# Kernel tuning notes

Measured on AMD Instinct MI355X. Metric: run time of the kernel, lower is better.

Reference implementation:

```python
import jax, jax.numpy as jnp
import numpy as np

B, T, H, C = 128, 1024, 512, 10


def setup_inputs() -> dict:
    key = jax.random.key(0)
    ks = jax.random.split(key, 8)
    s = 1.0 / np.sqrt(H)  # PyTorch LSTMCell/Linear default init scale
    return {
        "x": jax.random.normal(ks[0], (B, T), jnp.float32),
        "w_ih": jax.random.uniform(ks[1], (4 * H, 1), jnp.float32, -s, s),
        "w_hh": jax.random.uniform(ks[2], (4 * H, H), jnp.float32, -s, s),
        "b_ih": jax.random.uniform(ks[3], (4 * H,), jnp.float32, -s, s),
        "b_hh": jax.random.uniform(ks[4], (4 * H,), jnp.float32, -s, s),
        "w_t": jax.random.normal(ks[5], (2 * H, 1), jnp.float32) * 0.02,
        "w_fc": jax.random.uniform(ks[6], (C, H), jnp.float32, -s, s),
        "b_fc": jax.random.uniform(ks[7], (C,), jnp.float32, -s, s),
    }


def reference(x, w_ih, w_hh, b_ih, b_hh, w_t, w_fc, b_fc):
    # x: [B, T] scalar-per-step sequence (input_size == 1 in the original)
    Bz = x.shape[0]
    Hh = w_hh.shape[1]
    w1 = w_t[:Hh, 0]   # multiplies the new hidden h_t       [H]
    w2 = w_t[Hh:, 0]   # multiplies each history state h_j   [H]
    bias = b_ih + b_hh
    wih_row = w_ih[:, 0]  # [4H], since input_size == 1

    # Original computes, at step i, attn_c = sum_{j<=i} ((h_new@w1 + h_j@w2) * h_j)
    # over history [h_init=0, h_1, ..., h_i]. We keep running sums:
    #   S1 = sum_j h_j,   S2 = sum_j (h_j@w2) * h_j
    # so attn_c = (h_new@w1) * S1 + S2  -- identical math, O(T) instead of O(T^2).
    def step(carry, x_t):
        h, c, S1, S2 = carry
        gates = x_t[:, None] * wih_row[None, :] + h @ w_hh.T + bias  # [B,4H]
        i_g, f_g, g_g, o_g = jnp.split(gates, 4, axis=1)  # PyTorch gate order i,f,g,o
        c_new = jax.nn.sigmoid(f_g) * c + jax.nn.sigmoid(i_g) * jnp.tanh(g_g)
        h_new = jax.nn.sigmoid(o_g) * jnp.tanh(c_new)
        a = (h_new @ w1)[:, None]          # [B,1]
        attn = a * S1 + S2                 # [B,H]
        S1 = S1 + h_new
        S2 = S2 + (h_new @ w2)[:, None] * h_new
        return (h_new, c_new, S1, S2), (h_new, attn)

    z = jnp.zeros((Bz, Hh), x.dtype)
    _, (hs, attns) = jax.lax.scan(step, (z, z, z, z), x.T)  # [T,B,H] each
    out = jnp.transpose(hs + attns, (1, 0, 2))               # [B,T,H]
    return out @ w_fc.T + b_fc                               # [B,T,C]
```

## Files before the change

### kernel.cpp

```cpp
#include <hip/hip_runtime.h>
#include <math.h>

typedef __attribute__((ext_vector_type(8))) short bf16x8;
typedef __attribute__((ext_vector_type(4))) float f32x4;

static constexpr int Tt = 1024;
static constexpr int Hh = 512;
static constexpr int Cc = 10;

static constexpr int NXCD = 8;
static constexpr int BPX  = 32;
static constexpr int UPB  = 16;
static constexpr int NB   = 16;
static constexpr int THREADS = 256;
static constexpr int GRID = 256;

static constexpr size_t WS_HHI_B = 4096;
static constexpr size_t WS_HLO_B = 4096 + 32768;

__device__ __forceinline__ unsigned short f2bf(float f) {
    unsigned u = __builtin_bit_cast(unsigned, f);
    return (unsigned short)((u + 0x7FFFu + ((u >> 16) & 1u)) >> 16);
}
__device__ __forceinline__ float bf2f(unsigned short h) {
    unsigned u = ((unsigned)h) << 16;
    return __builtin_bit_cast(float, u);
}
__device__ __forceinline__ float dot4(float4 a, float4 b) {
    return a.x * b.x + a.y * b.y + a.z * b.z + a.w * b.w;
}
__device__ __forceinline__ float fsig(float x) {
    const float e = __builtin_amdgcn_exp2f(x * -1.44269504f);
    return __builtin_amdgcn_rcpf(1.0f + e);
}
__device__ __forceinline__ float ftanh(float x) {
    const float e = __builtin_amdgcn_exp2f(x * -2.88539008f);
    return 2.0f * __builtin_amdgcn_rcpf(1.0f + e) - 1.0f;
}

__global__ __launch_bounds__(THREADS, 1)
void lstm_fused(const float* __restrict__ x,
                const float* __restrict__ w_ih,
                const float* __restrict__ w_hh,
                const float* __restrict__ b_ih,
                const float* __restrict__ b_hh,
                const float* __restrict__ w_t,
                const float* __restrict__ w_fc,
                const float* __restrict__ b_fc,
                float* __restrict__ out,
                float* __restrict__ ws)
{
    const int tid  = threadIdx.x;
    const int lane = tid & 63;
    const int wv   = tid >> 6;

    int* flags    = (int*)ws;
    int* counters = (int*)ws + 256;
    unsigned short* hg_hi = (unsigned short*)((char*)ws + WS_HHI_B);
    unsigned short* hg_lo = (unsigned short*)((char*)ws + WS_HLO_B);

    __shared__ __align__(16) short wls_hi[64 * 512];
    __shared__ __align__(16) short wls_lo[64 * 512];
    __shared__ __align__(16) short hhi_ls[16 * 512];
    __shared__ __align__(16) short hlo_ls[16 * 512];
    float* gbuf = (float*)hhi_ls;
    int*   xchg = (int*)hlo_ls;

    if (tid == 0) {
        int xr;
        asm volatile("s_getreg_b32 %0, hwreg(20, 0, 32)" : "=s"(xr));
        const int xcd = xr & 7;
        xchg[0] = xcd;
        xchg[1] = atomicAdd(&counters[xcd * 32], 1) & 31;
    }
    __syncthreads();
    const int xcd  = xchg[0];
    const int rank = xchg[1];
    __syncthreads();
    const int fbase = xcd * BPX;

    {
        #pragma unroll
        for (int it = 0; it < 16; ++it) {
            const int idx = it * 256 + tid;
            const int lr = idx >> 6, kg = idx & 63;
            const int grow = (lr >> 4) * Hh + rank * UPB + (lr & 15);
            const float4* src = (const float4*)(w_hh + (size_t)grow * Hh + kg * 8);
            const float4 f0 = src[0], f1 = src[1];
            const float f[8] = { f0.x, f0.y, f0.z, f0.w, f1.x, f1.y, f1.z, f1.w };
            bf16x8 vhi, vlo;
            #pragma unroll
            for (int j = 0; j < 8; ++j) {
                const unsigned short h = f2bf(f[j]);
                vhi[j] = (short)h;
                vlo[j] = (short)f2bf(f[j] - bf2f(h));
            }
            const int off = (lr * 1024 + kg * 16) ^ ((lr & 7) << 4);
            *(bf16x8*)((char*)wls_hi + off) = vhi;
            *(bf16x8*)((char*)wls_lo + off) = vlo;
        }
    }

    const int u  = tid & 15;
    const int b_ = tid >> 4;
    const int gj = rank * UPB + u;
    const int gb = xcd * NB + b_;
    float wih_r[4], bias_r[4];
    #pragma unroll
    for (int g = 0; g < 4; ++g) {
        wih_r[g]  = w_ih[g * Hh + gj];
        bias_r[g] = b_ih[g * Hh + gj] + b_hh[g * Hh + gj];
    }
    float creg = 0.0f;

    const bool owner = (rank < NB);
    const int  gb_own = xcd * NB + rank;
    float S1w[Cc], S2w[Cc], bfc_r[Cc];
    #pragma unroll
    for (int c = 0; c < Cc; ++c) { S1w[c] = 0.f; S2w[c] = 0.f; bfc_r[c] = b_fc[c]; }

    const int arow  = wv * 16 + (lane & 15);
    const int aoff0 = arow * 1024 + ((lane >> 4) << 4);
    const int boff0 = (lane & 15) * 1024 + ((lane >> 4) << 4);
    const int xmask = (lane & 7) << 4;

    for (int t = 0; t <= Tt; ++t) {
        const int rb = t & 1, wb = rb ^ 1;

        if (t == 0) {
            const bf16x8 z = { 0, 0, 0, 0, 0, 0, 0, 0 };
            #pragma unroll
            for (int it = 0; it < 4; ++it) {
                const int idx = it * 256 + tid;
                const int row = idx >> 6, kg = idx & 63;
                const int off = (row * 1024 + kg * 16) ^ ((row & 7) << 4);
                *(bf16x8*)((char*)hhi_ls + off) = z;
                *(bf16x8*)((char*)hlo_ls + off) = z;
            }
        } else if (t < Tt) {
            const bf16x8* shi = (const bf16x8*)(hg_hi + (size_t)(rb * NXCD + xcd) * NB * Hh);
            const bf16x8* slo = (const bf16x8*)(hg_lo + (size_t)(rb * NXCD + xcd) * NB * Hh);
            #pragma unroll
            for (int it = 0; it < 4; ++it) {
                const int idx = it * 256 + tid;
                const int row = idx >> 6, kg = idx & 63;
                const bf16x8 vhi = shi[idx];
                const bf16x8 vlo = slo[idx];
                const int off = (row * 1024 + kg * 16) ^ ((row & 7) << 4);
                *(bf16x8*)((char*)hhi_ls + off) = vhi;
                *(bf16x8*)((char*)hlo_ls + off) = vlo;
            }
        }

        if (t > 0 && wv == 0 && owner) {
            const size_t rbase = ((size_t)(rb * NXCD + xcd) * NB + rank) * Hh + lane * 8;
            const bf16x8 vh = *(const bf16x8*)(hg_hi + rbase);
            const bf16x8 vl = *(const bf16x8*)(hg_lo + rbase);
            float f[8];
            #pragma unroll
            for (int j = 0; j < 8; ++j)
                f[j] = bf2f((unsigned short)vh[j]) + bf2f((unsigned short)vl[j]);
            const float4 hA = make_float4(f[0], f[1], f[2], f[3]);
            const float4 hB = make_float4(f[4], f[5], f[6], f[7]);
            const float4* wt4 = (const float4*)w_t;
            const float4* wf4 = (const float4*)w_fc;
            float r[12];
            r[0] = dot4(hA, wt4[lane * 2])       + dot4(hB, wt4[lane * 2 + 1]);
            r[1] = dot4(hA, wt4[128 + lane * 2]) + dot4(hB, wt4[128 + lane * 2 + 1]);
            #pragma unroll
            for (int c = 0; c < Cc; ++c)
                r[2 + c] = dot4(hA, wf4[c * 128 + lane * 2])
                         + dot4(hB, wf4[c * 128 + lane * 2 + 1]);
            #pragma unroll
            for (int m = 1; m <= 32; m <<= 1)
                #pragma unroll
                for (int k2 = 0; k2 < 12; ++k2)
                    r[k2] += __shfl_xor(r[k2], m, 64);

            if (lane == 0) {
                const float a = r[0], b2 = r[1];
                float* po = out + ((size_t)gb_own * Tt + (t - 1)) * Cc;
                #pragma unroll
                for (int c = 0; c < Cc; ++c) {
                    const float hw = r[2 + c];
                    po[c] = hw + a * S1w[c] + S2w[c] + bfc_r[c];
                    S1w[c] += hw;
                    S2w[c] += b2 * hw;
                }
            }
        }
        if (t == Tt) break;

        const float xv = x[(size_t)gb * Tt + t];
        __syncthreads();

        f32x4 acc0 = { 0.f, 0.f, 0.f, 0.f };
        f32x4 acc1 = { 0.f, 0.f, 0.f, 0.f };
        f32x4 acc2 = { 0.f, 0.f, 0.f, 0.f };
        #pragma unroll
        for (int kk = 0; kk < 16; ++kk) {
            const int ao = (aoff0 + kk * 64) ^ xmask;
            const int bo = (boff0 + kk * 64) ^ xmask;
            const bf16x8 ahi = *(const bf16x8*)((const char*)wls_hi + ao);
            const bf16x8 alo = *(const bf16x8*)((const char*)wls_lo + ao);
            const bf16x8 bhi = *(const bf16x8*)((const char*)hhi_ls + bo);
            const bf16x8 blo = *(const bf16x8*)((const char*)hlo_ls + bo);
            acc0 = __builtin_amdgcn_mfma_f32_16x16x32_bf16(ahi, bhi, acc0, 0, 0, 0);
            acc1 = __builtin_amdgcn_mfma_f32_16x16x32_bf16(ahi, blo, acc1, 0, 0, 0);
            acc2 = __builtin_amdgcn_mfma_f32_16x16x32_bf16(alo, bhi, acc2, 0, 0, 0);
        }
        __syncthreads();

        {
            const int unit0 = (lane >> 4) * 4;
            const int batch = lane & 15;
            #pragma unroll
            for (int r = 0; r < 4; ++r)
                gbuf[(wv * 16 + unit0 + r) * 20 + batch] = acc0[r] + acc1[r] + acc2[r];
        }
        __syncthreads();

        {
            const float gi = gbuf[(0 * UPB + u) * 20 + b_] + xv * wih_r[0] + bias_r[0];
            const float gf = gbuf[(1 * UPB + u) * 20 + b_] + xv * wih_r[1] + bias_r[1];
            const float gg = gbuf[(2 * UPB + u) * 20 + b_] + xv * wih_r[2] + bias_r[2];
            const float go = gbuf[(3 * UPB + u) * 20 + b_] + xv * wih_r[3] + bias_r[3];
            creg = fsig(gf) * creg + fsig(gi) * ftanh(gg);
            const float hnew = fsig(go) * ftanh(creg);
            const unsigned short hb = f2bf(hnew);
            const unsigned short lb = f2bf(hnew - bf2f(hb));
            const size_t hoff = ((size_t)(wb * NXCD + xcd) * NB + b_) * Hh + gj;
            hg_hi[hoff] = hb;
            hg_lo[hoff] = lb;
        }
        __syncthreads();

        if (tid == 0)
            *(volatile int*)(flags + fbase + rank) = t + 1;

        if (tid < 32) {
            const volatile int* fl = (const volatile int*)(flags + fbase + tid);
            int v = *fl;
            while (__any(v < t + 1)) {
                __builtin_amdgcn_s_sleep(1);
                asm volatile("buffer_inv\n\ts_waitcnt vmcnt(0)" ::: "memory");
                v = *fl;
            }
            asm volatile("buffer_inv\n\ts_waitcnt vmcnt(0)" ::: "memory");
        }
        __syncthreads();
    }
}

extern "C" void kernel_launch(void* const* d_in, const int* in_sizes, int n_in,
                              void* d_out, int out_size, void* d_ws, size_t ws_size,
                              hipStream_t stream)
{
    const float* xp  = (const float*)d_in[0];
    const float* wih = (const float*)d_in[1];
    const float* whh = (const float*)d_in[2];
    const float* bih = (const float*)d_in[3];
    const float* bhh = (const float*)d_in[4];
    const float* wt  = (const float*)d_in[5];
    const float* wfc = (const float*)d_in[6];
    const float* bfc = (const float*)d_in[7];
    float* outp = (float*)d_out;
    float* ws   = (float*)d_ws;

    (void)hipMemsetAsync(d_ws, 0, 4096, stream);

    hipLaunchKernelGGL(lstm_fused, dim3(GRID), dim3(THREADS), 0, stream,
                       xp, wih, whh, bih, bhh, wt, wfc, bfc, outp, ws);
}
```

Baseline: 4.424 ms.

## Hold recurrent weights in registers with 8 waves splitting K, double-buffer h in LDS

The recurrent weight slice (hi/lo bf16 split) now lives in VGPRs across 8 waves instead of in LDS. Each wave covers two gate tiles over a quarter of K, and the four partial sums are reduced through LDS. The h staging buffer is double-buffered and one barrier per step is removed, aiming to cut LDS traffic and per-step latency on the serial recurrence. In exchange, register pressure rises and the cross-wave partial-sum reduction adds work. The workspace offset for the lo buffer also grows.

```diff
diff --git a/kernel.cpp b/kernel.cpp
--- a/kernel.cpp
+++ b/kernel.cpp
@@ -12,11 +12,11 @@
 static constexpr int BPX  = 32;
 static constexpr int UPB  = 16;
 static constexpr int NB   = 16;
-static constexpr int THREADS = 256;
+static constexpr int THREADS = 512;
 static constexpr int GRID = 256;
 
 static constexpr size_t WS_HHI_B = 4096;
-static constexpr size_t WS_HLO_B = 4096 + 32768;
+static constexpr size_t WS_HLO_B = 4096 + 262144;
 
 __device__ __forceinline__ unsigned short f2bf(float f) {
     unsigned u = __builtin_bit_cast(unsigned, f);
@@ -38,7 +38,7 @@
     return 2.0f * __builtin_amdgcn_rcpf(1.0f + e) - 1.0f;
 }
 
-__global__ __launch_bounds__(THREADS, 1)
+__global__ __launch_bounds__(THREADS, 2)
 void lstm_fused(const float* __restrict__ x,
                 const float* __restrict__ w_ih,
                 const float* __restrict__ w_hh,
@@ -50,21 +50,23 @@
                 float* __restrict__ out,
                 float* __restrict__ ws)
 {
-    const int tid  = threadIdx.x;
-    const int lane = tid & 63;
-    const int wv   = tid >> 6;
+    const int tid   = threadIdx.x;
+    const int lane  = tid & 63;
+    const int wv    = tid >> 6;
+    const int mpair = wv & 1;
+    const int kq    = wv >> 1;
+    const int frow  = lane & 15;
+    const int kgrp  = lane >> 4;
 
     int* flags    = (int*)ws;
     int* counters = (int*)ws + 256;
     unsigned short* hg_hi = (unsigned short*)((char*)ws + WS_HHI_B);
     unsigned short* hg_lo = (unsigned short*)((char*)ws + WS_HLO_B);
 
-    __shared__ __align__(16) short wls_hi[64 * 512];
-    __shared__ __align__(16) short wls_lo[64 * 512];
-    __shared__ __align__(16) short hhi_ls[16 * 512];
-    __shared__ __align__(16) short hlo_ls[16 * 512];
-    float* gbuf = (float*)hhi_ls;
-    int*   xchg = (int*)hlo_ls;
+    __shared__ __align__(16) short hhi_ls[2][16 * 512];
+    __shared__ __align__(16) short hlo_ls[2][16 * 512];
+    __shared__ __align__(16) float gbuf[4 * 64 * 20];
+    int* xchg = (int*)gbuf;
 
     if (tid == 0) {
         int xr;
@@ -79,30 +81,30 @@
     __syncthreads();
     const int fbase = xcd * BPX;
 
-    {
+    bf16x8 wahi[2][4], walo[2][4];
+    #pragma unroll
+    for (int mt = 0; mt < 2; ++mt) {
+        const int gate = mpair * 2 + mt;
+        const float* wr = w_hh + (size_t)(gate * Hh + rank * UPB + frow) * Hh;
         #pragma unroll
-        for (int it = 0; it < 16; ++it) {
-            const int idx = it * 256 + tid;
-            const int lr = idx >> 6, kg = idx & 63;
-            const int grow = (lr >> 4) * Hh + rank * UPB + (lr & 15);
-            const float4* src = (const float4*)(w_hh + (size_t)grow * Hh + kg * 8);
-            const float4 f0 = src[0], f1 = src[1];
+        for (int kk = 0; kk < 4; ++kk) {
+            const float4* s = (const float4*)(wr + (kq * 4 + kk) * 32 + kgrp * 8);
+            const float4 f0 = s[0], f1 = s[1];
             const float f[8] = { f0.x, f0.y, f0.z, f0.w, f1.x, f1.y, f1.z, f1.w };
             bf16x8 vhi, vlo;
             #pragma unroll
             for (int j = 0; j < 8; ++j) {
-                const unsigned short h = f2bf(f[j]);
-                vhi[j] = (short)h;
-                vlo[j] = (short)f2bf(f[j] - bf2f(h));
-            }
-            const int off = (lr * 1024 + kg * 16) ^ ((lr & 7) << 4);
-            *(bf16x8*)((char*)wls_hi + off) = vhi;
-            *(bf16x8*)((char*)wls_lo + off) = vlo;
+                const unsigned short hb = f2bf(f[j]);
+                vhi[j] = (short)hb;
+                vlo[j] = (short)f2bf(f[j] - bf2f(hb));
+            }
+            wahi[mt][kk] = vhi;
+            walo[mt][kk] = vlo;
         }
     }
 
     const int u  = tid & 15;
-    const int b_ = tid >> 4;
+    const int b_ = (tid >> 4) & 15;
     const int gj = rank * UPB + u;
     const int gb = xcd * NB + b_;
     float wih_r[4], bias_r[4];
@@ -119,36 +121,33 @@
     #pragma unroll
     for (int c = 0; c < Cc; ++c) { S1w[c] = 0.f; S2w[c] = 0.f; bfc_r[c] = b_fc[c]; }
 
-    const int arow  = wv * 16 + (lane & 15);
-    const int aoff0 = arow * 1024 + ((lane >> 4) << 4);
-    const int boff0 = (lane & 15) * 1024 + ((lane >> 4) << 4);
-    const int xmask = (lane & 7) << 4;
-
     for (int t = 0; t <= Tt; ++t) {
         const int rb = t & 1, wb = rb ^ 1;
+        char* Lhi = (char*)hhi_ls[rb];
+        char* Llo = (char*)hlo_ls[rb];
 
         if (t == 0) {
             const bf16x8 z = { 0, 0, 0, 0, 0, 0, 0, 0 };
             #pragma unroll
-            for (int it = 0; it < 4; ++it) {
-                const int idx = it * 256 + tid;
+            for (int it = 0; it < 2; ++it) {
+                const int idx = it * 512 + tid;
                 const int row = idx >> 6, kg = idx & 63;
                 const int off = (row * 1024 + kg * 16) ^ ((row & 7) << 4);
-                *(bf16x8*)((char*)hhi_ls + off) = z;
-                *(bf16x8*)((char*)hlo_ls + off) = z;
+                *(bf16x8*)(Lhi + off) = z;
+                *(bf16x8*)(Llo + off) = z;
             }
         } else if (t < Tt) {
             const bf16x8* shi = (const bf16x8*)(hg_hi + (size_t)(rb * NXCD + xcd) * NB * Hh);
             const bf16x8* slo = (const bf16x8*)(hg_lo + (size_t)(rb * NXCD + xcd) * NB * Hh);
             #pragma unroll
-            for (int it = 0; it < 4; ++it) {
-                const int idx = it * 256 + tid;
+            for (int it = 0; it < 2; ++it) {
+                const int idx = it * 512 + tid;
                 const int row = idx >> 6, kg = idx & 63;
                 const bf16x8 vhi = shi[idx];
                 const bf16x8 vlo = slo[idx];
                 const int off = (row * 1024 + kg * 16) ^ ((row & 7) << 4);
-                *(bf16x8*)((char*)hhi_ls + off) = vhi;
-                *(bf16x8*)((char*)hlo_ls + off) = vlo;
+                *(bf16x8*)(Lhi + off) = vhi;
+                *(bf16x8*)(Llo + off) = vlo;
             }
         }
 
@@ -191,47 +190,62 @@
         }
         if (t == Tt) break;
 
-        const float xv = x[(size_t)gb * Tt + t];
-        __syncthreads();
-
-        f32x4 acc0 = { 0.f, 0.f, 0.f, 0.f };
-        f32x4 acc1 = { 0.f, 0.f, 0.f, 0.f };
-        f32x4 acc2 = { 0.f, 0.f, 0.f, 0.f };
+        float xv = 0.f;
+        if (tid < 256) xv = x[(size_t)gb * Tt + t];
+        __syncthreads();
+
+        f32x4 acc[2][3];
         #pragma unroll
-        for (int kk = 0; kk < 16; ++kk) {
-            const int ao = (aoff0 + kk * 64) ^ xmask;
-            const int bo = (boff0 + kk * 64) ^ xmask;
-            const bf16x8 ahi = *(const bf16x8*)((const char*)wls_hi + ao);
-            const bf16x8 alo = *(const bf16x8*)((const char*)wls_lo + ao);
-            const bf16x8 bhi = *(const bf16x8*)((const char*)hhi_ls + bo);
-            const bf16x8 blo = *(const bf16x8*)((const char*)hlo_ls + bo);
-            acc0 = __builtin_amdgcn_mfma_f32_16x16x32_bf16(ahi, bhi, acc0, 0, 0, 0);
-            acc1 = __builtin_amdgcn_mfma_f32_16x16x32_bf16(ahi, blo, acc1, 0, 0, 0);
-            acc2 = __builtin_amdgcn_mfma_f32_16x16x32_bf16(alo, bhi, acc2, 0, 0, 0);
-        }
-        __syncthreads();
-
+        for (int mt = 0; mt < 2; ++mt)
+            #pragma unroll
+            for (int p = 0; p < 3; ++p)
+                acc[mt][p] = f32x4{ 0.f, 0.f, 0.f, 0.f };
+
+        #pragma unroll
+        for (int kk = 0; kk < 4; ++kk) {
+            const int kabs = kq * 4 + kk;
+            const int bo = (frow * 1024 + kgrp * 16 + kabs * 64) ^ ((lane & 7) << 4);
+            const bf16x8 bhi = *(const bf16x8*)(Lhi + bo);
+            const bf16x8 blo = *(const bf16x8*)(Llo + bo);
+            #pragma unroll
+            for (int mt = 0; mt < 2; ++mt) {
+                acc[mt][0] = __builtin_amdgcn_mfma_f32_16x16x32_bf16(wahi[mt][kk], bhi, acc[mt][0], 0, 0, 0);
+                acc[mt][1] = __builtin_amdgcn_mfma_f32_16x16x32_bf16(wahi[mt][kk], blo, acc[mt][1], 0, 0, 0);
+                acc[mt][2] = __builtin_amdgcn_mfma_f32_16x16x32_bf16(walo[mt][kk], bhi, acc[mt][2], 0, 0, 0);
+            }
+        }
         {
-            const int unit0 = (lane >> 4) * 4;
-            const int batch = lane & 15;
-            #pragma unroll
-            for (int r = 0; r < 4; ++r)
-                gbuf[(wv * 16 + unit0 + r) * 20 + batch] = acc0[r] + acc1[r] + acc2[r];
-        }
-        __syncthreads();
-
-        {
-            const float gi = gbuf[(0 * UPB + u) * 20 + b_] + xv * wih_r[0] + bias_r[0];
-            const float gf = gbuf[(1 * UPB + u) * 20 + b_] + xv * wih_r[1] + bias_r[1];
-            const float gg = gbuf[(2 * UPB + u) * 20 + b_] + xv * wih_r[2] + bias_r[2];
-            const float go = gbuf[(3 * UPB + u) * 20 + b_] + xv * wih_r[3] + bias_r[3];
+            const int u0 = kgrp * 4;
+            #pragma unroll
+            for (int mt = 0; mt < 2; ++mt) {
+                const int g = mpair * 2 + mt;
+                #pragma unroll
+                for (int r = 0; r < 4; ++r)
+                    gbuf[(kq * 64 + g * 16 + u0 + r) * 20 + frow] =
+                        acc[mt][0][r] + acc[mt][1][r] + acc[mt][2][r];
+            }
+        }
+        __syncthreads();
+
+        if (tid < 256) {
+            float gs[4];
+            #pragma unroll
+            for (int g = 0; g < 4; ++g) {
+                const int base = (g * 16 + u) * 20 + b_;
+                gs[g] = gbuf[base] + gbuf[base + 1280]
+                      + gbuf[base + 2560] + gbuf[base + 3840];
+            }
+            const float gi = gs[0] + xv * wih_r[0] + bias_r[0];
+            const float gf = gs[1] + xv * wih_r[1] + bias_r[1];
+            const float gg = gs[2] + xv * wih_r[2] + bias_r[2];
+            const float go = gs[3] + xv * wih_r[3] + bias_r[3];
             creg = fsig(gf) * creg + fsig(gi) * ftanh(gg);
             const float hnew = fsig(go) * ftanh(creg);
-            const unsigned short hb = f2bf(hnew);
-            const unsigned short lb = f2bf(hnew - bf2f(hb));
+            const unsigned short hb2 = f2bf(hnew);
+            const unsigned short lb2 = f2bf(hnew - bf2f(hb2));
             const size_t hoff = ((size_t)(wb * NXCD + xcd) * NB + b_) * Hh + gj;
-            hg_hi[hoff] = hb;
-            hg_lo[hoff] = lb;
+            hg_hi[hoff] = hb2;
+            hg_lo[hoff] = lb2;
         }
         __syncthreads();
 
```

After: 5.254 ms. +18.8%, slower.
